# Performance work log

Measured on AMD Instinct MI355X. Metric: run time of the kernel, lower is better.

The kernel has to match this reference:

```python
import jax, jax.numpy as jnp
import numpy as np

GROUP_SIZE = 128
# AWQ nibble unpack order: reverse_awq_order = [0,4,1,5,2,6,3,7]; shifts = order*4
AWQ_SHIFTS = jnp.array([0, 16, 4, 20, 8, 24, 12, 28], dtype=jnp.int32)


def awq_dequantize(qweight, scales, qzeros, group_size=GROUP_SIZE):
    # qweight: [K, N//8] int32, scales: [K//g, N] f32, qzeros: [K//g, N//8] int32
    K = qweight.shape[0]
    N = scales.shape[1]
    # unpack 8 4-bit values per int32 in AWQ order -> [K, N]
    w = ((qweight[:, :, None] >> AWQ_SHIFTS) & 15).reshape(K, N).astype(scales.dtype)
    z = ((qzeros[:, :, None] >> AWQ_SHIFTS) & 15).reshape(-1, N).astype(scales.dtype)
    # broadcast per-group scales/zeros along the K (row) axis
    z_full = jnp.repeat(z, group_size, axis=0)       # [K, N]
    s_full = jnp.repeat(scales, group_size, axis=0)  # [K, N]
    return (w - z_full) * s_full                      # [K, N]


def setup_inputs() -> dict:
    key = jax.random.key(0)
    k1, k2, k3, k4 = jax.random.split(key, 4)
    K, N, g = 4096, 11008, GROUP_SIZE
    x = jax.random.normal(k1, (4096, K), dtype=jnp.float32)
    qweight = jax.random.randint(k2, (K, N // 8), 0, 2147483647, dtype=jnp.int32)
    scales = jax.random.uniform(k3, (K // g, N), dtype=jnp.float32) * 0.01
    qzeros = jax.random.randint(k4, (K // g, N // 8), 0, 2147483647, dtype=jnp.int32)
    return {"x": x, "qweight": qweight, "scales": scales, "qzeros": qzeros}


def reference(x, qweight, scales, qzeros):
    # F.linear(x, W_deq.T) == x @ W_deq, W_deq: [K, N]
    w_deq = awq_dequantize(qweight, scales, qzeros)
    return x @ w_deq  # [tokens, N]
```

## Files before the change

### kernel.cpp

```cpp
#include <hip/hip_runtime.h>
#include <hip/hip_fp16.h>
#include <stdint.h>
#include <stddef.h>

#define MM 4096
#define NN 11008
#define KK 4096
#define NQ (NN / 8)

#define BM 256
#define BN 256
#define BK 64
#define NKT (KK / BK)
#define GRID_N (NN / BN)
#define GRID_M (MM / BM)
#define NWG (GRID_N * GRID_M)

#define HT 8192

typedef _Float16 half8 __attribute__((ext_vector_type(8)));
typedef _Float16 half2v __attribute__((ext_vector_type(2)));
typedef float f32x4 __attribute__((ext_vector_type(4)));
typedef uint32_t uint4v __attribute__((ext_vector_type(4)));

union U1H2 { uint32_t u; half2v h; };
union U4H8 { uint4v u; half8 h; };

__device__ __forceinline__ void gload_lds16(const void* g, void* l) {
  __builtin_amdgcn_global_load_lds(
      (const __attribute__((address_space(1))) uint32_t*)g,
      (__attribute__((address_space(3))) uint32_t*)l, 16, 0, 0);
}

__global__ __launch_bounds__(256) void convert_x_kernel(const float* __restrict__ x,
                                                        _Float16* __restrict__ xh) {
  const int idx = (blockIdx.x * 256 + threadIdx.x) * 8;
  const float4* p = reinterpret_cast<const float4*>(x + idx);
  float4 a = p[0], b = p[1];
  U4H8 r;
  r.h[0] = (_Float16)a.x; r.h[1] = (_Float16)a.y;
  r.h[2] = (_Float16)a.z; r.h[3] = (_Float16)a.w;
  r.h[4] = (_Float16)b.x; r.h[5] = (_Float16)b.y;
  r.h[6] = (_Float16)b.z; r.h[7] = (_Float16)b.w;
  *reinterpret_cast<uint4v*>(xh + idx) = r.u;
}

__global__ __launch_bounds__(256) void dequant_w_kernel(const uint32_t* __restrict__ qw,
                                                        const float* __restrict__ sc,
                                                        const uint32_t* __restrict__ qz,
                                                        _Float16* __restrict__ w1) {
  const int T = blockIdx.x * 256 + threadIdx.x;
  const int qc = T % NQ;
  const int kb8 = T / NQ;
  const int g = kb8 >> 4;

  const uint32_t* qp = qw + (size_t)(kb8 * 8) * NQ + qc;
  uint32_t q[8];
#pragma unroll
  for (int j = 0; j < 8; ++j) q[j] = qp[(size_t)j * NQ];

  const uint32_t zq = qz[(size_t)g * NQ + qc];
  const float* sp = sc + (size_t)g * NN + qc * 8;
  float4 s0 = *reinterpret_cast<const float4*>(sp);
  float4 s1 = *reinterpret_cast<const float4*>(sp + 4);
  const float sv[8] = {s0.x, s0.y, s0.z, s0.w, s1.x, s1.y, s1.z, s1.w};

  _Float16* op = w1 + ((size_t)kb8 * NN + (size_t)qc * 8) * 8;
#pragma unroll
  for (int c = 0; c < 8; ++c) {
    const int sh = ((c >> 1) << 2) + ((c & 1) << 4);
    uint32_t zc = ((zq >> sh) & 15u) | 0x6400u;
    zc |= zc << 16;
    U1H2 uz; uz.u = zc;
    const _Float16 hs = (_Float16)sv[c];
    half2v s2 = {hs, hs};
    uint4v outp;
#pragma unroll
    for (int i = 0; i < 4; ++i) {
      const uint32_t lo = (q[2 * i] >> sh) & 15u;
      const uint32_t hi = (q[2 * i + 1] >> sh) & 15u;
      U1H2 uw; uw.u = lo | (hi << 16) | 0x64006400u;
      U1H2 ur; ur.h = (uw.h - uz.h) * s2;
      outp[i] = ur.u;
    }
    *reinterpret_cast<uint4v*>(op + c * 8) = outp;
  }
}

__global__ __launch_bounds__(512, 2)
void gemm_pipe(const _Float16* __restrict__ xh, const _Float16* __restrict__ w1,
               float* __restrict__ out) {
  __shared__ __align__(16) _Float16 S[65536];

  const int tid = threadIdx.x;
  const int lane = tid & 63;
  const int wid = tid >> 6;
  const int wm = wid >> 2;
  const int wn = wid & 3;
  const int lr = lane & 15;
  const int lq = lane >> 4;

  const int wg = blockIdx.x;
  const int xcd = wg & 7;
  const int j = wg >> 3;
  const int m0 = (xcd * 2 + (j & 1)) * BM;
  const int n0 = (j >> 1) * BN;

  const int c0 = tid, c1 = 512 + tid;
  const _Float16* aS0 = xh + (size_t)(m0 + (c0 >> 2)) * KK
                           + ((c0 & 3) ^ ((c0 >> 3) & 3)) * 8;
  const _Float16* aS1 = xh + (size_t)(m0 + (c1 >> 2)) * KK
                           + ((c1 & 3) ^ ((c1 >> 3) & 3)) * 8;
  const _Float16* bS0 = w1 + ((size_t)(c0 >> 8) * NN + n0 + (c0 & 255)) * 8;
  const _Float16* bS1 = w1 + ((size_t)(c1 >> 8) * NN + n0 + (c1 & 255)) * 8;

  const int sa8 = (lq ^ ((lr >> 1) & 3)) * 8;
  const int vA = (wm * 128 + lr) * 32 + sa8;
  const int vB = lq * 2048 + (wn * 64 + lr) * 8;

  f32x4 acc[8][4];
  const f32x4 fz = {0.f, 0.f, 0.f, 0.f};
#pragma unroll
  for (int i = 0; i < 8; ++i)
#pragma unroll
    for (int jn = 0; jn < 4; ++jn) acc[i][jn] = fz;

  half8 af[4], bf[4], bf2[4];

#define RD_A4(BUF, KKX, MIH)                                                   \
  _Pragma("unroll") for (int mi = 0; mi < 4; ++mi)                             \
      af[mi] = *reinterpret_cast<const half8*>(                                \
          &S[((BUF) * 2 + (KKX)) * HT + ((MIH) + mi) * 512 + vA]);

#define RD_B4(BUF, KKX, REG)                                                   \
  _Pragma("unroll") for (int ni = 0; ni < 4; ++ni)                             \
      REG[ni] = *reinterpret_cast<const half8*>(                               \
          &S[32768 + ((BUF) * 2 + (KKX)) * HT + ni * 128 + vB]);

#define MF16(ACCH, REG)                                                        \
  _Pragma("unroll") for (int mi = 0; mi < 4; ++mi)                             \
      _Pragma("unroll") for (int ni = 0; ni < 4; ++ni)                         \
          acc[(ACCH) + mi][ni] = __builtin_amdgcn_mfma_f32_16x16x32_f16(       \
              af[mi], REG[ni], acc[(ACCH) + mi][ni], 0, 0, 0);

#define STG_A(KKX, BUFX, AOFF)                                                 \
  gload_lds16(aS0 + (AOFF) + (KKX) * 32,                                       \
              &S[((BUFX) * 2 + (KKX)) * HT + wid * 512]);                      \
  gload_lds16(aS1 + (AOFF) + (KKX) * 32,                                       \
              &S[((BUFX) * 2 + (KKX)) * HT + 4096 + wid * 512]);

#define STG_B(KKX, BUFX, BOFF)                                                 \
  gload_lds16(bS0 + (BOFF) + (size_t)(KKX) * NN * 32,                          \
              &S[32768 + ((BUFX) * 2 + (KKX)) * HT + wid * 512]);              \
  gload_lds16(bS1 + (BOFF) + (size_t)(KKX) * NN * 32,                          \
              &S[32768 + ((BUFX) * 2 + (KKX)) * HT + 4096 + wid * 512]);

#define BARRIER __builtin_amdgcn_s_barrier()
#define LGKM0 asm volatile("s_waitcnt lgkmcnt(0)" ::: "memory")
#define VMC(N) asm volatile("s_waitcnt vmcnt(" #N ")" ::: "memory")
#define SB0 __builtin_amdgcn_sched_barrier(0)
#define PRIO1 __builtin_amdgcn_s_setprio(1)
#define PRIO0 __builtin_amdgcn_s_setprio(0)

#define TILE64(T, BUF)                                                         \
  {                                                                            \
    const size_t aOff = (size_t)(((T) + 1) & (NKT - 1)) * BK;                  \
    const size_t bOff = (size_t)(((T) + 1) & (NKT - 1)) * ((size_t)NN * 64);   \
                                                                       \
    RD_A4(BUF, 0, 0)                                                           \
    RD_B4(BUF, 0, bf)                                                          \
    STG_A(0, (BUF) ^ 1, aOff)                                                  \
    BARRIER; LGKM0; SB0;                                                       \
    PRIO1; MF16(0, bf) PRIO0;                                                  \
    BARRIER; SB0;                                                              \
                                                                       \
    RD_A4(BUF, 0, 4)                                                           \
    STG_B(0, (BUF) ^ 1, bOff)                                                  \
    VMC(6); BARRIER; LGKM0; SB0;                                               \
    PRIO1; MF16(4, bf) PRIO0;                                                  \
    BARRIER; SB0;                                                              \
                                                                       \
    RD_A4(BUF, 1, 0)                                                           \
    RD_B4(BUF, 1, bf2)                                                         \
    STG_A(1, (BUF) ^ 1, aOff)                                                  \
    VMC(6); BARRIER; LGKM0; SB0;                                               \
    PRIO1; MF16(0, bf2) PRIO0;                                                 \
    BARRIER; SB0;                                                              \
                                                                       \
    RD_A4(BUF, 1, 4)                                                           \
    STG_B(1, (BUF) ^ 1, bOff)                                                  \
    VMC(4); BARRIER; LGKM0; SB0;                                               \
    PRIO1; MF16(4, bf2) PRIO0;                                                 \
    BARRIER; SB0;                                                              \
  }

  STG_A(0, 0, 0)
  STG_B(0, 0, 0)
  STG_A(1, 0, 0)
  STG_B(1, 0, 0)
  VMC(4);
  BARRIER; SB0;

  for (int it = 0; it < NKT / 2; ++it) {
    const int t0 = it * 2;
    TILE64(t0, 0)
    TILE64(t0 + 1, 1)
  }

#undef TILE64
#undef RD_A4
#undef RD_B4
#undef MF16
#undef STG_A
#undef STG_B

  float* op = out + (size_t)(m0 + wm * 128) * NN + (n0 + wn * 64);
#pragma unroll
  for (int mi = 0; mi < 8; ++mi)
#pragma unroll
    for (int ni = 0; ni < 4; ++ni)
#pragma unroll
      for (int i = 0; i < 4; ++i) {
        const int row = mi * 16 + lq * 4 + i;
        const int col = ni * 16 + lr;
        op[(size_t)row * NN + col] = acc[mi][ni][i];
      }
}

template <bool APRE>
__global__ __launch_bounds__(256)
void awq_gemm(const float* __restrict__ x, const _Float16* __restrict__ xh,
              const uint32_t* __restrict__ qw, const float* __restrict__ sc,
              const uint32_t* __restrict__ qz, float* __restrict__ out) {
  __shared__ __align__(16) _Float16 Asf[128 * 64];
  __shared__ __align__(16) _Float16 Bsf[128 * 64];

  const int tid = threadIdx.x;
  const int lane = tid & 63;
  const int wid = tid >> 6;
  const int wr = wid >> 1;
  const int wc = wid & 1;
  const int n0 = blockIdx.x * 128;
  const int m0 = blockIdx.y * 128;
  const int lr = lane & 15;
  const int lq = lane >> 4;

  const int bn = tid & 127;
  const int bh = tid >> 7;
  const int gn = n0 + bn;
  const int qc = gn >> 3;
  const int jj = gn & 7;
  const int shift = ((jj >> 1) << 2) + ((jj & 1) << 4);

  const int ar = tid >> 1;
  const int ah = tid & 1;

  f32x4 acc[4][4];
  const f32x4 fz = {0.f, 0.f, 0.f, 0.f};
#pragma unroll
  for (int i = 0; i < 4; ++i)
#pragma unroll
    for (int jn = 0; jn < 4; ++jn) acc[i][jn] = fz;

  half2v zsp = {(_Float16)0.f, (_Float16)0.f};
  half2v ssp = {(_Float16)0.f, (_Float16)0.f};

  for (int kt = 0; kt < KK / 64; ++kt) {
    const int k0 = kt * 64;
    if ((kt & 1) == 0) {
      const int g = k0 >> 7;
      const uint32_t zq = qz[(size_t)g * NQ + qc];
      uint32_t zm = ((zq >> shift) & 15u) | 0x6400u;
      zm |= zm << 16;
      U1H2 uz; uz.u = zm; zsp = uz.h;
      const float s = sc[(size_t)g * NN + gn];
      const _Float16 hs = (_Float16)s;
      ssp[0] = hs; ssp[1] = hs;
    }
    __syncthreads();
    if (APRE) {
#pragma unroll
      for (int i = 0; i < 4; ++i) {
        const int cbase = (i * 4 + wid) * 64;
        const int chunk = cbase + lane;
        const int mrow = chunk >> 3;
        const int slot = (chunk & 7) ^ (mrow & 7);
        const _Float16* gp = xh + (size_t)(m0 + mrow) * KK + k0 + slot * 8;
        gload_lds16(gp, (void*)&Asf[cbase * 8]);
      }
    } else {
      const float* xp = x + (size_t)(m0 + ar) * KK + k0 + ah * 32;
#pragma unroll
      for (int j2 = 0; j2 < 4; ++j2) {
        float4 a4 = *reinterpret_cast<const float4*>(xp + j2 * 8);
        float4 b4 = *reinterpret_cast<const float4*>(xp + j2 * 8 + 4);
        U4H8 r;
        r.h[0] = (_Float16)a4.x; r.h[1] = (_Float16)a4.y;
        r.h[2] = (_Float16)a4.z; r.h[3] = (_Float16)a4.w;
        r.h[4] = (_Float16)b4.x; r.h[5] = (_Float16)b4.y;
        r.h[6] = (_Float16)b4.z; r.h[7] = (_Float16)b4.w;
        const int slot = (ah * 4 + j2) ^ (ar & 7);
        *reinterpret_cast<uint4v*>(&Asf[ar * 64 + slot * 8]) = r.u;
      }
    }
    {
      const uint32_t* qp = qw + (size_t)(k0 + bh * 32) * NQ + qc;
#pragma unroll
      for (int f = 0; f < 4; ++f) {
        uint32_t qv[8];
#pragma unroll
        for (int jv = 0; jv < 8; ++jv) qv[jv] = qp[(size_t)(f * 8 + jv) * NQ];
        uint4v wp;
#pragma unroll
        for (int p = 0; p < 4; ++p) {
          const uint32_t lo = (qv[2 * p] >> shift) & 15u;
          const uint32_t hi = (qv[2 * p + 1] >> shift);
          const uint32_t w01 = (((hi << 16) | lo) & 0x000F000Fu) | 0x64006400u;
          U1H2 uw; uw.u = w01;
          U1H2 ur; ur.h = (uw.h - zsp) * ssp;
          wp[p] = ur.u;
        }
        const int slot = (bh * 4 + f) ^ (bn & 7);
        *reinterpret_cast<uint4v*>(&Bsf[bn * 64 + slot * 8]) = wp;
      }
    }
    __syncthreads();
#pragma unroll
    for (int kq = 0; kq < 2; ++kq) {
      half8 af[4], bf[4];
#pragma unroll
      for (int mi = 0; mi < 4; ++mi) {
        const int am = wr * 64 + mi * 16 + lr;
        const int aslot = (kq * 4 + lq) ^ (am & 7);
        af[mi] = *reinterpret_cast<const half8*>(&Asf[am * 64 + aslot * 8]);
      }
#pragma unroll
      for (int ni = 0; ni < 4; ++ni) {
        const int bn2 = wc * 64 + ni * 16 + lr;
        const int bslot = (kq * 4 + lq) ^ (bn2 & 7);
        bf[ni] = *reinterpret_cast<const half8*>(&Bsf[bn2 * 64 + bslot * 8]);
      }
#pragma unroll
      for (int mi = 0; mi < 4; ++mi)
#pragma unroll
        for (int ni = 0; ni < 4; ++ni)
          acc[mi][ni] = __builtin_amdgcn_mfma_f32_16x16x32_f16(af[mi], bf[ni], acc[mi][ni], 0, 0, 0);
    }
  }

  float* op = out + (size_t)(m0 + wr * 64) * NN + (n0 + wc * 64);
#pragma unroll
  for (int mi = 0; mi < 4; ++mi)
#pragma unroll
    for (int ni = 0; ni < 4; ++ni)
#pragma unroll
      for (int i = 0; i < 4; ++i) {
        const int row = mi * 16 + lq * 4 + i;
        const int col = ni * 16 + lr;
        op[(size_t)row * NN + col] = acc[mi][ni][i];
      }
}

extern "C" void kernel_launch(void* const* d_in, const int* in_sizes, int n_in,
                              void* d_out, int out_size, void* d_ws, size_t ws_size,
                              hipStream_t stream) {
  const float* x = (const float*)d_in[0];
  const uint32_t* qw = (const uint32_t*)d_in[1];
  const float* sc = (const float*)d_in[2];
  const uint32_t* qz = (const uint32_t*)d_in[3];
  float* out = (float*)d_out;

  const size_t xh_bytes = (size_t)MM * KK * sizeof(_Float16);
  const size_t w1_bytes = (size_t)KK * NN * sizeof(_Float16);

  if (ws_size >= xh_bytes + w1_bytes) {
    _Float16* xh = (_Float16*)d_ws;
    _Float16* w1 = (_Float16*)((char*)d_ws + xh_bytes);
    convert_x_kernel<<<(MM * KK) / (256 * 8), 256, 0, stream>>>(x, xh);
    dequant_w_kernel<<<(KK / 8) * NQ / 256, 256, 0, stream>>>(qw, sc, qz, w1);
    gemm_pipe<<<NWG, 512, 0, stream>>>(xh, w1, out);
  } else if (ws_size >= xh_bytes) {
    _Float16* xh = (_Float16*)d_ws;
    convert_x_kernel<<<(MM * KK) / (256 * 8), 256, 0, stream>>>(x, xh);
    awq_gemm<true><<<dim3(NN / 128, MM / 128), 256, 0, stream>>>(x, xh, qw, sc, qz, out);
  } else {
    awq_gemm<false><<<dim3(NN / 128, MM / 128), 256, 0, stream>>>(x, nullptr, qw, sc, qz, out);
  }
}
```

Before: 389.7 us.

## Double-buffer MFMA fragment registers to overlap LDS reads with MFMA

```diff
diff --git a/kernel.cpp b/kernel.cpp
--- a/kernel.cpp
+++ b/kernel.cpp
@@ -125,23 +125,23 @@
 #pragma unroll
     for (int jn = 0; jn < 4; ++jn) acc[i][jn] = fz;
 
-  half8 af[4], bf[4], bf2[4];
-
-#define RD_A4(BUF, KKX, MIH)                                                   \
+  half8 af0[4], af1[4], bf0[4], bf1[4];
+
+#define RD_A4(DST, BUF, KKX, MIH)                                              \
   _Pragma("unroll") for (int mi = 0; mi < 4; ++mi)                             \
-      af[mi] = *reinterpret_cast<const half8*>(                                \
+      DST[mi] = *reinterpret_cast<const half8*>(                               \
           &S[((BUF) * 2 + (KKX)) * HT + ((MIH) + mi) * 512 + vA]);
 
-#define RD_B4(BUF, KKX, REG)                                                   \
+#define RD_B4(DST, BUF, KKX)                                                   \
   _Pragma("unroll") for (int ni = 0; ni < 4; ++ni)                             \
-      REG[ni] = *reinterpret_cast<const half8*>(                               \
+      DST[ni] = *reinterpret_cast<const half8*>(                               \
           &S[32768 + ((BUF) * 2 + (KKX)) * HT + ni * 128 + vB]);
 
-#define MF16(ACCH, REG)                                                        \
+#define MF16(ACCH, AREG, BREG)                                                 \
   _Pragma("unroll") for (int mi = 0; mi < 4; ++mi)                             \
       _Pragma("unroll") for (int ni = 0; ni < 4; ++ni)                         \
           acc[(ACCH) + mi][ni] = __builtin_amdgcn_mfma_f32_16x16x32_f16(       \
-              af[mi], REG[ni], acc[(ACCH) + mi][ni], 0, 0, 0);
+              AREG[mi], BREG[ni], acc[(ACCH) + mi][ni], 0, 0, 0);
 
 #define STG_A(KKX, BUFX, AOFF)                                                 \
   gload_lds16(aS0 + (AOFF) + (KKX) * 32,                                       \
@@ -156,58 +156,79 @@
               &S[32768 + ((BUFX) * 2 + (KKX)) * HT + 4096 + wid * 512]);
 
 #define BARRIER __builtin_amdgcn_s_barrier()
-#define LGKM0 asm volatile("s_waitcnt lgkmcnt(0)" ::: "memory")
+#define LGKM(N) asm volatile("s_waitcnt lgkmcnt(" #N ")" ::: "memory")
 #define VMC(N) asm volatile("s_waitcnt vmcnt(" #N ")" ::: "memory")
 #define SB0 __builtin_amdgcn_sched_barrier(0)
 #define PRIO1 __builtin_amdgcn_s_setprio(1)
 #define PRIO0 __builtin_amdgcn_s_setprio(0)
 
-#define TILE64(T, BUF)                                                         \
-  {                                                                            \
-    const size_t aOff = (size_t)(((T) + 1) & (NKT - 1)) * BK;                  \
-    const size_t bOff = (size_t)(((T) + 1) & (NKT - 1)) * ((size_t)NN * 64);   \
-                                                                       \
-    RD_A4(BUF, 0, 0)                                                           \
-    RD_B4(BUF, 0, bf)                                                          \
-    STG_A(0, (BUF) ^ 1, aOff)                                                  \
-    BARRIER; LGKM0; SB0;                                                       \
-    PRIO1; MF16(0, bf) PRIO0;                                                  \
-    BARRIER; SB0;                                                              \
-                                                                       \
-    RD_A4(BUF, 0, 4)                                                           \
-    STG_B(0, (BUF) ^ 1, bOff)                                                  \
-    VMC(6); BARRIER; LGKM0; SB0;                                               \
-    PRIO1; MF16(4, bf) PRIO0;                                                  \
-    BARRIER; SB0;                                                              \
-                                                                       \
-    RD_A4(BUF, 1, 0)                                                           \
-    RD_B4(BUF, 1, bf2)                                                         \
-    STG_A(1, (BUF) ^ 1, aOff)                                                  \
-    VMC(6); BARRIER; LGKM0; SB0;                                               \
-    PRIO1; MF16(0, bf2) PRIO0;                                                 \
-    BARRIER; SB0;                                                              \
-                                                                       \
-    RD_A4(BUF, 1, 4)                                                           \
-    STG_B(1, (BUF) ^ 1, bOff)                                                  \
-    VMC(4); BARRIER; LGKM0; SB0;                                               \
-    PRIO1; MF16(4, bf2) PRIO0;                                                 \
-    BARRIER; SB0;                                                              \
-  }
-
   STG_A(0, 0, 0)
   STG_B(0, 0, 0)
+  VMC(0);
+  BARRIER; SB0;
+  RD_A4(af0, 0, 0, 0)
+  RD_B4(bf0, 0, 0)
   STG_A(1, 0, 0)
   STG_B(1, 0, 0)
-  VMC(4);
-  BARRIER; SB0;
 
   for (int it = 0; it < NKT / 2; ++it) {
     const int t0 = it * 2;
-    TILE64(t0, 0)
-    TILE64(t0 + 1, 1)
+    const size_t aO1 = (size_t)((t0 + 1) & (NKT - 1)) * BK;
+    const size_t bO1 = (size_t)((t0 + 1) & (NKT - 1)) * ((size_t)NN * 64);
+    const size_t aO2 = (size_t)((t0 + 2) & (NKT - 1)) * BK;
+    const size_t bO2 = (size_t)((t0 + 2) & (NKT - 1)) * ((size_t)NN * 64);
+
+    BARRIER; SB0;
+    RD_A4(af1, 0, 0, 4)
+    STG_A(0, 1, aO1)
+    LGKM(4); SB0;
+    PRIO1; MF16(0, af0, bf0) PRIO0;
+    VMC(2);
+    BARRIER; SB0;
+    RD_A4(af0, 0, 1, 0)
+    RD_B4(bf1, 0, 1)
+    STG_B(0, 1, bO1)
+    LGKM(8); SB0;
+    PRIO1; MF16(4, af1, bf0) PRIO0;
+    BARRIER; SB0;
+    RD_A4(af1, 0, 1, 4)
+    STG_A(1, 1, aO1)
+    LGKM(4); SB0;
+    PRIO1; MF16(0, af0, bf1) PRIO0;
+    VMC(2);
+    BARRIER; SB0;
+    RD_A4(af0, 1, 0, 0)
+    RD_B4(bf0, 1, 0)
+    STG_B(1, 1, bO1)
+    LGKM(8); SB0;
+    PRIO1; MF16(4, af1, bf1) PRIO0;
+
+    BARRIER; SB0;
+    RD_A4(af1, 1, 0, 4)
+    STG_A(0, 0, aO2)
+    LGKM(4); SB0;
+    PRIO1; MF16(0, af0, bf0) PRIO0;
+    VMC(2);
+    BARRIER; SB0;
+    RD_A4(af0, 1, 1, 0)
+    RD_B4(bf1, 1, 1)
+    STG_B(0, 0, bO2)
+    LGKM(8); SB0;
+    PRIO1; MF16(4, af1, bf0) PRIO0;
+    BARRIER; SB0;
+    RD_A4(af1, 1, 1, 4)
+    STG_A(1, 0, aO2)
+    LGKM(4); SB0;
+    PRIO1; MF16(0, af0, bf1) PRIO0;
+    VMC(2);
+    BARRIER; SB0;
+    RD_A4(af0, 0, 0, 0)
+    RD_B4(bf0, 0, 0)
+    STG_B(1, 0, bO2)
+    LGKM(8); SB0;
+    PRIO1; MF16(4, af1, bf1) PRIO0;
   }
 
-#undef TILE64
 #undef RD_A4
 #undef RD_B4
 #undef MF16
```

Measured after the change: 382.6 us, median of 2. Within noise of the previous version (-1.8%).

## Switch GEMM to 32x32x16 MFMA with triple-buffered BK=32 LDS pipeline

Applied to the files above, without the earlier changes.

```diff
diff --git a/kernel.cpp b/kernel.cpp
--- a/kernel.cpp
+++ b/kernel.cpp
@@ -10,16 +10,15 @@
 
 #define BM 256
 #define BN 256
-#define BK 64
+#define BK 32
 #define NKT (KK / BK)
 #define GRID_N (NN / BN)
 #define GRID_M (MM / BM)
 #define NWG (GRID_N * GRID_M)
 
-#define HT 8192
-
 typedef _Float16 half8 __attribute__((ext_vector_type(8)));
 typedef _Float16 half2v __attribute__((ext_vector_type(2)));
+typedef float f32x16 __attribute__((ext_vector_type(16)));
 typedef float f32x4 __attribute__((ext_vector_type(4)));
 typedef uint32_t uint4v __attribute__((ext_vector_type(4)));
 
@@ -90,15 +89,15 @@
 __global__ __launch_bounds__(512, 2)
 void gemm_pipe(const _Float16* __restrict__ xh, const _Float16* __restrict__ w1,
                float* __restrict__ out) {
-  __shared__ __align__(16) _Float16 S[65536];
+  __shared__ __align__(16) _Float16 S[49152];
 
   const int tid = threadIdx.x;
   const int lane = tid & 63;
   const int wid = tid >> 6;
   const int wm = wid >> 2;
   const int wn = wid & 3;
-  const int lr = lane & 15;
-  const int lq = lane >> 4;
+  const int l31 = lane & 31;
+  const int lh = lane >> 5;
 
   const int wg = blockIdx.x;
   const int xcd = wg & 7;
@@ -107,124 +106,123 @@
   const int n0 = (j >> 1) * BN;
 
   const int c0 = tid, c1 = 512 + tid;
-  const _Float16* aS0 = xh + (size_t)(m0 + (c0 >> 2)) * KK
-                           + ((c0 & 3) ^ ((c0 >> 3) & 3)) * 8;
-  const _Float16* aS1 = xh + (size_t)(m0 + (c1 >> 2)) * KK
-                           + ((c1 & 3) ^ ((c1 >> 3) & 3)) * 8;
+  const int rr0 = c0 >> 3, sd0 = (c0 & 7) ^ (rr0 & 7);
+  const int rw0 = 2 * rr0 + (sd0 >> 2), uk0 = sd0 & 3;
+  const int rr1 = c1 >> 3, sd1 = (c1 & 7) ^ (rr1 & 7);
+  const int rw1 = 2 * rr1 + (sd1 >> 2), uk1 = sd1 & 3;
+  const _Float16* aS0 = xh + (size_t)(m0 + rw0) * KK + uk0 * 8;
+  const _Float16* aS1 = xh + (size_t)(m0 + rw1) * KK + uk1 * 8;
   const _Float16* bS0 = w1 + ((size_t)(c0 >> 8) * NN + n0 + (c0 & 255)) * 8;
   const _Float16* bS1 = w1 + ((size_t)(c1 >> 8) * NN + n0 + (c1 & 255)) * 8;
 
-  const int sa8 = (lq ^ ((lr >> 1) & 3)) * 8;
-  const int vA = (wm * 128 + lr) * 32 + sa8;
-  const int vB = lq * 2048 + (wn * 64 + lr) * 8;
-
-  f32x4 acc[8][4];
-  const f32x4 fz = {0.f, 0.f, 0.f, 0.f};
+  const int x7 = (lane >> 1) & 7;
+  const int p4 = (lane & 1) * 4;
+  const int sa0 = (p4 + lh) ^ x7;
+  const int sa1 = (p4 + 2 + lh) ^ x7;
+  const int rrL = l31 >> 1;
+  const int vA0 = (wm * 64 + rrL) * 64 + sa0 * 8;
+  const int vA1 = (wm * 64 + rrL) * 64 + sa1 * 8;
+  const int vB0 = lh * 2048 + (wn * 64 + l31) * 8;
+  const int vB1 = vB0 + 4096;
+
+  f32x16 acc[8];
 #pragma unroll
   for (int i = 0; i < 8; ++i)
 #pragma unroll
-    for (int jn = 0; jn < 4; ++jn) acc[i][jn] = fz;
-
-  half8 af[4], bf[4], bf2[4];
-
-#define RD_A4(BUF, KKX, MIH)                                                   \
-  _Pragma("unroll") for (int mi = 0; mi < 4; ++mi)                             \
-      af[mi] = *reinterpret_cast<const half8*>(                                \
-          &S[((BUF) * 2 + (KKX)) * HT + ((MIH) + mi) * 512 + vA]);
-
-#define RD_B4(BUF, KKX, REG)                                                   \
-  _Pragma("unroll") for (int ni = 0; ni < 4; ++ni)                             \
-      REG[ni] = *reinterpret_cast<const half8*>(                               \
-          &S[32768 + ((BUF) * 2 + (KKX)) * HT + ni * 128 + vB]);
-
-#define MF16(ACCH, REG)                                                        \
-  _Pragma("unroll") for (int mi = 0; mi < 4; ++mi)                             \
-      _Pragma("unroll") for (int ni = 0; ni < 4; ++ni)                         \
-          acc[(ACCH) + mi][ni] = __builtin_amdgcn_mfma_f32_16x16x32_f16(       \
-              af[mi], REG[ni], acc[(ACCH) + mi][ni], 0, 0, 0);
-
-#define STG_A(KKX, BUFX, AOFF)                                                 \
-  gload_lds16(aS0 + (AOFF) + (KKX) * 32,                                       \
-              &S[((BUFX) * 2 + (KKX)) * HT + wid * 512]);                      \
-  gload_lds16(aS1 + (AOFF) + (KKX) * 32,                                       \
-              &S[((BUFX) * 2 + (KKX)) * HT + 4096 + wid * 512]);
-
-#define STG_B(KKX, BUFX, BOFF)                                                 \
-  gload_lds16(bS0 + (BOFF) + (size_t)(KKX) * NN * 32,                          \
-              &S[32768 + ((BUFX) * 2 + (KKX)) * HT + wid * 512]);              \
-  gload_lds16(bS1 + (BOFF) + (size_t)(KKX) * NN * 32,                          \
-              &S[32768 + ((BUFX) * 2 + (KKX)) * HT + 4096 + wid * 512]);
+    for (int e = 0; e < 16; ++e) acc[i][e] = 0.f;
+
+  half8 af0[4], af1[4], bf0[2], bf1[2];
+
+#define RD_A(DST, U, VAX)                                                      \
+  _Pragma("unroll") for (int mb = 0; mb < 4; ++mb)                             \
+      DST[mb] = *reinterpret_cast<const half8*>(                               \
+          &S[(U) * 8192 + mb * 1024 + (VAX)]);
+
+#define RD_B(DST, U, VBX)                                                      \
+  _Pragma("unroll") for (int nb = 0; nb < 2; ++nb)                             \
+      DST[nb] = *reinterpret_cast<const half8*>(                               \
+          &S[24576 + (U) * 8192 + nb * 256 + (VBX)]);
+
+#define MFMA8(AREG, BREG)                                                      \
+  _Pragma("unroll") for (int mb = 0; mb < 4; ++mb)                             \
+      _Pragma("unroll") for (int nb = 0; nb < 2; ++nb)                         \
+          acc[mb * 2 + nb] = __builtin_amdgcn_mfma_f32_32x32x16_f16(           \
+              AREG[mb], BREG[nb], acc[mb * 2 + nb], 0, 0, 0);
+
+#define STG_A(U, TOFF)                                                         \
+  gload_lds16(aS0 + (size_t)(TOFF) * BK, &S[(U) * 8192 + wid * 512]);          \
+  gload_lds16(aS1 + (size_t)(TOFF) * BK, &S[(U) * 8192 + 4096 + wid * 512]);
+
+#define STG_B(U, TOFF)                                                         \
+  gload_lds16(bS0 + (size_t)(TOFF) * NN * 32,                                  \
+              &S[24576 + (U) * 8192 + wid * 512]);                             \
+  gload_lds16(bS1 + (size_t)(TOFF) * NN * 32,                                  \
+              &S[24576 + (U) * 8192 + 4096 + wid * 512]);
 
 #define BARRIER __builtin_amdgcn_s_barrier()
-#define LGKM0 asm volatile("s_waitcnt lgkmcnt(0)" ::: "memory")
+#define LGKM(N) asm volatile("s_waitcnt lgkmcnt(" #N ")" ::: "memory")
 #define VMC(N) asm volatile("s_waitcnt vmcnt(" #N ")" ::: "memory")
 #define SB0 __builtin_amdgcn_sched_barrier(0)
 #define PRIO1 __builtin_amdgcn_s_setprio(1)
 #define PRIO0 __builtin_amdgcn_s_setprio(0)
 
-#define TILE64(T, BUF)                                                         \
+#define TILE(T, U0, U1, U2)                                                    \
   {                                                                            \
-    const size_t aOff = (size_t)(((T) + 1) & (NKT - 1)) * BK;                  \
-    const size_t bOff = (size_t)(((T) + 1) & (NKT - 1)) * ((size_t)NN * 64);   \
-                                                                       \
-    RD_A4(BUF, 0, 0)                                                           \
-    RD_B4(BUF, 0, bf)                                                          \
-    STG_A(0, (BUF) ^ 1, aOff)                                                  \
-    BARRIER; LGKM0; SB0;                                                       \
-    PRIO1; MF16(0, bf) PRIO0;                                                  \
+          \
     BARRIER; SB0;                                                              \
-                                                                       \
-    RD_A4(BUF, 0, 4)                                                           \
-    STG_B(0, (BUF) ^ 1, bOff)                                                  \
-    VMC(6); BARRIER; LGKM0; SB0;                                               \
-    PRIO1; MF16(4, bf) PRIO0;                                                  \
+    RD_A(af1, U0, vA1)                                                         \
+    RD_B(bf1, U0, vB1)                                                         \
+    STG_A(U2, ((T) + 2) & (NKT - 1))                                           \
+    LGKM(6); SB0;                                                              \
+    PRIO1; MFMA8(af0, bf0) PRIO0;                                              \
+    VMC(2);                                                                    \
+            \
     BARRIER; SB0;                                                              \
-                                                                       \
-    RD_A4(BUF, 1, 0)                                                           \
-    RD_B4(BUF, 1, bf2)                                                         \
-    STG_A(1, (BUF) ^ 1, aOff)                                                  \
-    VMC(6); BARRIER; LGKM0; SB0;                                               \
-    PRIO1; MF16(0, bf2) PRIO0;                                                 \
-    BARRIER; SB0;                                                              \
-                                                                       \
-    RD_A4(BUF, 1, 4)                                                           \
-    STG_B(1, (BUF) ^ 1, bOff)                                                  \
-    VMC(4); BARRIER; LGKM0; SB0;                                               \
-    PRIO1; MF16(4, bf2) PRIO0;                                                 \
-    BARRIER; SB0;                                                              \
-  }
-
-  STG_A(0, 0, 0)
-  STG_B(0, 0, 0)
-  STG_A(1, 0, 0)
-  STG_B(1, 0, 0)
+    RD_A(af0, U1, vA0)                                                         \
+    RD_B(bf0, U1, vB0)                                                         \
+    STG_B(U2, ((T) + 2) & (NKT - 1))                                           \
+    LGKM(6); SB0;                                                              \
+    PRIO1; MFMA8(af1, bf1) PRIO0;                                              \
+  }
+
+  STG_A(0, 0)
+  STG_B(0, 0)
+  STG_A(1, 1)
+  STG_B(1, 1)
   VMC(4);
   BARRIER; SB0;
-
-  for (int it = 0; it < NKT / 2; ++it) {
-    const int t0 = it * 2;
-    TILE64(t0, 0)
-    TILE64(t0 + 1, 1)
-  }
-
-#undef TILE64
-#undef RD_A4
-#undef RD_B4
-#undef MF16
+  RD_A(af0, 0, vA0)
+  RD_B(bf0, 0, vB0)
+
+  for (int it = 0; it < 42; ++it) {
+    const int t0 = it * 3;
+    TILE(t0, 0, 1, 2)
+    TILE(t0 + 1, 1, 2, 0)
+    TILE(t0 + 2, 2, 0, 1)
+  }
+  TILE(126, 0, 1, 2)
+  TILE(127, 1, 2, 0)
+
+#undef TILE
+#undef RD_A
+#undef RD_B
+#undef MFMA8
 #undef STG_A
 #undef STG_B
 
   float* op = out + (size_t)(m0 + wm * 128) * NN + (n0 + wn * 64);
 #pragma unroll
-  for (int mi = 0; mi < 8; ++mi)
-#pragma unroll
-    for (int ni = 0; ni < 4; ++ni)
-#pragma unroll
-      for (int i = 0; i < 4; ++i) {
-        const int row = mi * 16 + lq * 4 + i;
-        const int col = ni * 16 + lr;
-        op[(size_t)row * NN + col] = acc[mi][ni][i];
-      }
+  for (int mb = 0; mb < 4; ++mb)
+#pragma unroll
+    for (int nb = 0; nb < 2; ++nb)
+#pragma unroll
+      for (int g = 0; g < 4; ++g)
+#pragma unroll
+        for (int e = 0; e < 4; ++e) {
+          const int row = mb * 32 + 4 * lh + 8 * g + e;
+          const int col = nb * 32 + l31;
+          op[(size_t)row * NN + col] = acc[mb * 2 + nb][g * 4 + e];
+        }
 }
 
 template <bool APRE>
```

After: 417.1 us. 1.07x slower.
